# Kernel optimization log

Hardware: AMD Instinct MI355X
Metric: run time of the kernel (lower is better)

The kernel has to match this reference:

```python
import jax, jax.numpy as jnp
import numpy as np

H = 1024      # hidden_size
NH = 16       # num_attention_heads
DK = H // NH  # head dim
C = 1024      # cyclic_size


def setup_inputs() -> dict:
    key = jax.random.key(0)
    ks = jax.random.split(key, 13)
    B, S = 2, 2048
    s = 1.0 / np.sqrt(H)
    inp = {
        "q": jax.random.normal(ks[0], (B, S, H), jnp.float32),
        "k": jax.random.normal(ks[1], (B, S, H), jnp.float32),
        "v": jax.random.normal(ks[2], (B, S, H), jnp.float32),
        "Wq": jax.random.normal(ks[3], (H, H), jnp.float32) * s,
        "bq": jnp.zeros((H,), jnp.float32),
        "Wk": jax.random.normal(ks[4], (H, H), jnp.float32) * s,
        "bk": jnp.zeros((H,), jnp.float32),
        "Wv": jax.random.normal(ks[5], (H, H), jnp.float32) * s,
        "bv": jnp.zeros((H,), jnp.float32),
        "Wo": jax.random.normal(ks[6], (H, H), jnp.float32) * s,
        "bo": jnp.zeros((H,), jnp.float32),
        "Wc": jax.random.normal(ks[7], (H, C), jnp.float32) * s,
        "bc": jnp.zeros((C,), jnp.float32),
    }
    return inp


def _split_heads(x):
    B, S, _ = x.shape
    return x.reshape(B, S, NH, DK).transpose(0, 2, 1, 3)  # [B,NH,S,DK]


def reference(q, k, v, Wq, bq, Wk, bk, Wv, bv, Wo, bo, Wc, bc):
    Q = _split_heads(q @ Wq + bq)
    K = _split_heads(k @ Wk + bk)
    V = _split_heads(v @ Wv + bv)
    # unfused SDPA: full [B,NH,S,S] scores, as in the original module
    scores = jnp.einsum("bhqd,bhkd->bhqk", Q, K) / jnp.sqrt(jnp.float32(DK))
    probs = jax.nn.softmax(scores, axis=-1)
    attn = jnp.einsum("bhqk,bhkd->bhqd", probs, V)  # [B,NH,S,DK]
    B, _, S, _ = attn.shape
    merged = attn.transpose(0, 2, 1, 3).reshape(B, S, H)
    h = merged @ Wo + bo
    c = merged @ Wc + bc
    return (c, h)
```

## Files before the change

kernel.cpp:

```cpp
#include <hip/hip_runtime.h>
#include <stdint.h>

typedef unsigned short u16;
typedef short bf16x8 __attribute__((ext_vector_type(8)));
typedef short bf16x4 __attribute__((ext_vector_type(4)));
typedef float f32x4 __attribute__((ext_vector_type(4)));

#define MB (1u<<20)
#define CL2 0.18033688f

static __device__ __forceinline__ u16 f2bf(float x){
  union { float f; unsigned u; } v; v.f = x;
  return (u16)((v.u + 0x7FFFu + ((v.u >> 16) & 1u)) >> 16);
}

static __device__ __forceinline__ void gld_lds16(const void* g, void* l){
  __builtin_amdgcn_global_load_lds((const __attribute__((address_space(1))) unsigned int*)g,
                                   (__attribute__((address_space(3))) unsigned int*)l, 16, 0, 0);
}

__global__ void convx(const float* __restrict__ q, const float* __restrict__ k, const float* __restrict__ v,
                      u16* __restrict__ qb, u16* __restrict__ kb, u16* __restrict__ vb){
  const float* s = blockIdx.z==0 ? q : (blockIdx.z==1 ? k : v);
  u16* d = blockIdx.z==0 ? qb : (blockIdx.z==1 ? kb : vb);
  int i = (blockIdx.x*256 + threadIdx.x)*4;
  float4 f = *(const float4*)(s + i);
  ushort4 o; o.x=f2bf(f.x); o.y=f2bf(f.y); o.z=f2bf(f.z); o.w=f2bf(f.w);
  *(ushort4*)(d + i) = o;
}

__global__ void convw(const float* W0,const float* W1,const float* W2,const float* W3,const float* W4,
                      u16* T0,u16* T1,u16* T2,u16* T3,u16* T4){
  const float* W = blockIdx.z==0?W0:blockIdx.z==1?W1:blockIdx.z==2?W2:blockIdx.z==3?W3:W4;
  u16* T = blockIdx.z==0?T0:blockIdx.z==1?T1:blockIdx.z==2?T2:blockIdx.z==3?T3:T4;
  __shared__ u16 t[64][65];
  int k0 = blockIdx.x*64, n0 = blockIdx.y*64;
  for (int i=0;i<16;i++){
    int idx = i*256 + threadIdx.x;
    int r = idx >> 6, c = idx & 63;
    t[r][c] = f2bf(W[(size_t)(k0+r)*1024 + n0 + c]);
  }
  __syncthreads();
  for (int i=0;i<2;i++){
    int idx = i*256 + threadIdx.x;
    int nl = idx >> 3, kc = idx & 7;
    bf16x8 o;
    #pragma unroll
    for (int j=0;j<8;j++) o[j] = (short)t[kc*8+j][nl];
    *(bf16x8*)(T + (size_t)(n0+nl)*1024 + k0 + kc*8) = o;
  }
}

template<int MODE>
static __device__ __forceinline__ void gemm_bt_dev(const u16* __restrict__ A, const u16* __restrict__ Bt,
                                                   const float* __restrict__ bias, void* __restrict__ Cout){
  __shared__ u16 As[128*32];
  __shared__ u16 Bs[128*32];
  const int tid = threadIdx.x, lane = tid & 63, w = tid >> 6;
  const int wm = w >> 1, wn = w & 1, quad = lane >> 4, lr = lane & 15;
  const int m0 = blockIdx.y * 128, n0 = blockIdx.x * 128;
  f32x4 acc[4][4] = {};
  const u16* Ab = A + (size_t)m0*1024;
  const u16* Bb = Bt + (size_t)n0*1024;
  const int srow = w*16 + (lane>>2);
  const int sg   = (lane & 3);
  for (int k0 = 0; k0 < 1024; k0 += 32){
    #pragma unroll
    for (int r = 0; r < 2; ++r){
      int row = r*64 + srow;
      int g = sg ^ ((row>>1)&3);
      gld_lds16(Ab + (size_t)row*1024 + k0 + g*8, As + (r*64 + w*16)*32);
      gld_lds16(Bb + (size_t)row*1024 + k0 + g*8, Bs + (r*64 + w*16)*32);
    }
    __syncthreads();
    bf16x8 af[4], bfr[4];
    #pragma unroll
    for (int i=0;i<4;i++){
      int rowa = wm*64 + i*16 + lr;
      af[i] = *(const bf16x8*)(As + rowa*32 + ((quad ^ ((rowa>>1)&3))*8));
      int rowb = wn*64 + i*16 + lr;
      bfr[i] = *(const bf16x8*)(Bs + rowb*32 + ((quad ^ ((rowb>>1)&3))*8));
    }
    #pragma unroll
    for (int mi=0;mi<4;mi++)
      #pragma unroll
      for (int ni=0;ni<4;ni++)
        acc[mi][ni] = __builtin_amdgcn_mfma_f32_16x16x32_bf16(af[mi], bfr[ni], acc[mi][ni], 0, 0, 0);
    __syncthreads();
  }
  #pragma unroll
  for (int mi=0;mi<4;mi++){
    int row = m0 + wm*64 + mi*16 + quad*4;
    #pragma unroll
    for (int ni=0;ni<4;ni++){
      int col = n0 + wn*64 + ni*16 + lr;
      float bb = bias[col];
      #pragma unroll
      for (int rg=0; rg<4; rg++){
        float vv = acc[mi][ni][rg] + bb;
        int r = row + rg;
        if (MODE == 0){
          ((u16*)Cout)[(size_t)r*1024 + col] = f2bf(vv);
        } else if (MODE == 4){
          ((u16*)Cout)[(size_t)r*1024 + col] = f2bf(vv * CL2);
        } else if (MODE == 1){
          ((float*)Cout)[(size_t)r*1024 + col] = vv;
        } else if (MODE == 2){
          int b2 = r >> 11, s = r & 2047, kb2 = s >> 7, kvl = s & 127;
          int hh = col >> 6, hg = (col & 63) >> 3, hl = col & 7;
          ((u16*)Cout)[((size_t)(b2*16+hh)*16 + kb2)*8192 + hg*1024 + kvl*8 + hl] = f2bf(vv);
        } else {
          int b2 = r >> 11, s = r & 2047, kb2 = s >> 7, kvl = s & 127;
          int sgv = kvl >> 2, sl = kvl & 3;
          int hh = col >> 6, dd = col & 63;
          ((u16*)Cout)[((size_t)(b2*16+hh)*16 + kb2)*8192 + sgv*256 + dd*4 + sl] = f2bf(vv);
        }
      }
    }
  }
}

__global__ void qkv_gemm(const u16* qb,const u16* kb,const u16* vb,
                         const u16* Wqt,const u16* Wkt,const u16* Wvt,
                         const float* bq,const float* bk,const float* bv,
                         u16* Qb,u16* Kr,u16* Vr){
  if (blockIdx.z == 0)      gemm_bt_dev<4>(qb, Wqt, bq, Qb);
  else if (blockIdx.z == 1) gemm_bt_dev<2>(kb, Wkt, bk, Kr);
  else                      gemm_bt_dev<3>(vb, Wvt, bv, Vr);
}

__global__ void out_gemm(const u16* Mg, const u16* Wct, const u16* Wot,
                         const float* bc, const float* bo, float* out){
  const u16* B = blockIdx.z==0? Wct : Wot;
  const float* bias = blockIdx.z==0? bc : bo;
  float* C = out + (blockIdx.z==0? 0 : 4194304);
  gemm_bt_dev<1>(Mg, B, bias, C);
}

__global__ __launch_bounds__(512,4) void attn(const u16* __restrict__ Qb, const u16* __restrict__ Kr,
                                              const u16* __restrict__ Vr, u16* __restrict__ Mg){
  __shared__ u16 Ks[2][8192];
  __shared__ u16 Vs[2][8192];
  const int qt = blockIdx.x, bh = blockIdx.y, b = bh >> 4, h = bh & 15;
  const int tid = threadIdx.x, lane = tid & 63, w = tid >> 6;
  const int quad = lane >> 4, lr = lane & 15;
  const int q0 = qt*128 + w*16;

  bf16x8 aq[2];
  #pragma unroll
  for (int ks=0;ks<2;ks++)
    aq[ks] = *(const bf16x8*)(Qb + (size_t)(b*2048 + q0 + lr)*1024 + h*64 + ks*32 + quad*8);

  f32x4 acco[4] = {};
  float lsum = 0.f;

  const u16* Krb = Kr + (size_t)bh*131072;
  const u16* Vrb = Vr + (size_t)bh*131072;

  gld_lds16(Krb + tid*8,        &Ks[0][w*512]);
  gld_lds16(Krb + 4096 + tid*8, &Ks[0][4096 + w*512]);
  gld_lds16(Vrb + tid*8,        &Vs[0][w*512]);
  gld_lds16(Vrb + 4096 + tid*8, &Vs[0][4096 + w*512]);

  for (int kb = 0; kb < 16; kb++){
    __syncthreads();
    const int cur = kb & 1;
    if (kb < 15){
      const u16* kg = Krb + (size_t)(kb+1)*8192;
      const u16* vg = Vrb + (size_t)(kb+1)*8192;
      gld_lds16(kg + tid*8,        &Ks[cur^1][w*512]);
      gld_lds16(kg + 4096 + tid*8, &Ks[cur^1][4096 + w*512]);
      gld_lds16(vg + tid*8,        &Vs[cur^1][w*512]);
      gld_lds16(vg + 4096 + tid*8, &Vs[cur^1][4096 + w*512]);
    }
    const u16* Ksc = Ks[cur];
    const u16* Vsc = Vs[cur];

    f32x4 accs[8] = {};
    #pragma unroll
    for (int ks=0;ks<2;ks++){
      #pragma unroll
      for (int mt=0;mt<8;mt++){
        bf16x8 kf = *(const bf16x8*)(Ksc + (ks*4+quad)*1024 + (mt*16+lr)*8);
        accs[mt] = __builtin_amdgcn_mfma_f32_16x16x32_bf16(kf, aq[ks], accs[mt], 0,0,0);
      }
    }

    bf16x4 pf[8];
    f32x4 psum = {0.f,0.f,0.f,0.f};
    #pragma unroll
    for (int mt=0;mt<8;mt++){
      float p0 = __builtin_amdgcn_exp2f(accs[mt][0]);
      float p1 = __builtin_amdgcn_exp2f(accs[mt][1]);
      float p2 = __builtin_amdgcn_exp2f(accs[mt][2]);
      float p3 = __builtin_amdgcn_exp2f(accs[mt][3]);
      psum[0] += p0; psum[1] += p1; psum[2] += p2; psum[3] += p3;
      unsigned u0 = __float_as_uint(p0) + 0x8000u;
      unsigned u1 = __float_as_uint(p1) + 0x8000u;
      unsigned u2 = __float_as_uint(p2) + 0x8000u;
      unsigned u3 = __float_as_uint(p3) + 0x8000u;
      union { int2 i2; bf16x4 v; } pk;
      pk.i2.x = (int)__builtin_amdgcn_perm(u1, u0, 0x07060302u);
      pk.i2.y = (int)__builtin_amdgcn_perm(u3, u2, 0x07060302u);
      pf[mt] = pk.v;
    }
    lsum += (psum[0] + psum[1]) + (psum[2] + psum[3]);

    #pragma unroll
    for (int dt=0;dt<4;dt++){
      #pragma unroll
      for (int mt=0;mt<8;mt++){
        bf16x4 vf = *(const bf16x4*)(Vsc + (mt*4+quad)*256 + (dt*16+lr)*4);
        acco[dt] = __builtin_amdgcn_mfma_f32_16x16x16bf16_1k(vf, pf[mt], acco[dt], 0,0,0);
      }
    }
  }

  lsum += __shfl_xor(lsum, 16, 64);
  lsum += __shfl_xor(lsum, 32, 64);
  float inv = 1.f / lsum;

  u16* dst = Mg + (size_t)(b*2048 + q0 + lr)*1024 + h*64;
  #pragma unroll
  for (int dt=0;dt<4;dt++){
    bf16x4 o;
    #pragma unroll
    for (int rg=0;rg<4;rg++) o[rg] = (short)f2bf(acco[dt][rg]*inv);
    *(bf16x4*)(dst + dt*16 + quad*4) = o;
  }
}

extern "C" void kernel_launch(void* const* d_in, const int* in_sizes, int n_in,
                              void* d_out, int out_size, void* d_ws, size_t ws_size,
                              hipStream_t stream){
  const float* q  = (const float*)d_in[0];
  const float* k  = (const float*)d_in[1];
  const float* v  = (const float*)d_in[2];
  const float* Wq = (const float*)d_in[3];
  const float* bq = (const float*)d_in[4];
  const float* Wk = (const float*)d_in[5];
  const float* bk = (const float*)d_in[6];
  const float* Wv = (const float*)d_in[7];
  const float* bv = (const float*)d_in[8];
  const float* Wo = (const float*)d_in[9];
  const float* bo = (const float*)d_in[10];
  const float* Wc = (const float*)d_in[11];
  const float* bc = (const float*)d_in[12];
  char* ws = (char*)d_ws;
  u16* qb  = (u16*)(ws + (size_t)0*MB);
  u16* kb  = (u16*)(ws + (size_t)8*MB);
  u16* vb  = (u16*)(ws + (size_t)16*MB);
  u16* Wqt = (u16*)(ws + (size_t)24*MB);
  u16* Wkt = (u16*)(ws + (size_t)26*MB);
  u16* Wvt = (u16*)(ws + (size_t)28*MB);
  u16* Wot = (u16*)(ws + (size_t)30*MB);
  u16* Wct = (u16*)(ws + (size_t)32*MB);
  u16* Qb  = (u16*)(ws + (size_t)34*MB);
  u16* Kr  = (u16*)(ws + (size_t)42*MB);
  u16* Vr  = (u16*)(ws + (size_t)50*MB);
  u16* Mg  = (u16*)(ws + (size_t)58*MB);

  dim3 blk(256,1,1);
  hipLaunchKernelGGL(convx,    dim3(4096,1,3), blk, 0, stream, q,k,v, qb,kb,vb);
  hipLaunchKernelGGL(convw,    dim3(16,16,5),  blk, 0, stream, Wq,Wk,Wv,Wo,Wc, Wqt,Wkt,Wvt,Wot,Wct);
  hipLaunchKernelGGL(qkv_gemm, dim3(8,32,3),   blk, 0, stream, qb,kb,vb, Wqt,Wkt,Wvt, bq,bk,bv, Qb,Kr,Vr);
  hipLaunchKernelGGL(attn,     dim3(16,32,1),  dim3(512,1,1), 0, stream, Qb, Kr, Vr, Mg);
  hipLaunchKernelGGL(out_gemm, dim3(8,32,2),   blk, 0, stream, Mg, Wct, Wot, bc, bo, (float*)d_out);
}
```

Measured before the change: 247.6 us.

## Process two query tiles per wave in attention and sum rows via MFMA

The attention block shrinks from 512 to 256 threads, and each wave now handles 32 query rows as two 16-row tiles instead of one. Each K/V fragment read from shared memory therefore feeds twice as many MFMAs, halving LDS traffic per unit of work. The softmax row sum is no longer a VALU accumulation plus cross-lane shuffles; it comes from an extra MFMA against a vector of ones. The costs are higher register pressure and fewer waves per block to hide latency, and the MFMA row sum is taken over the bf16-rounded probabilities rather than the fp32 values.

```diff
diff --git a/kernel.cpp b/kernel.cpp
--- a/kernel.cpp
+++ b/kernel.cpp
@@ -137,30 +137,34 @@
   gemm_bt_dev<1>(Mg, B, bias, C);
 }
 
-__global__ __launch_bounds__(512,4) void attn(const u16* __restrict__ Qb, const u16* __restrict__ Kr,
+__global__ __launch_bounds__(256,2) void attn(const u16* __restrict__ Qb, const u16* __restrict__ Kr,
                                               const u16* __restrict__ Vr, u16* __restrict__ Mg){
   __shared__ u16 Ks[2][8192];
   __shared__ u16 Vs[2][8192];
   const int qt = blockIdx.x, bh = blockIdx.y, b = bh >> 4, h = bh & 15;
   const int tid = threadIdx.x, lane = tid & 63, w = tid >> 6;
   const int quad = lane >> 4, lr = lane & 15;
-  const int q0 = qt*128 + w*16;
-
-  bf16x8 aq[2];
-  #pragma unroll
-  for (int ks=0;ks<2;ks++)
-    aq[ks] = *(const bf16x8*)(Qb + (size_t)(b*2048 + q0 + lr)*1024 + h*64 + ks*32 + quad*8);
-
-  f32x4 acco[4] = {};
-  float lsum = 0.f;
+  const int q0 = qt*128 + w*32;
+
+  bf16x8 aq[2][2];
+  #pragma unroll
+  for (int t=0;t<2;t++)
+    #pragma unroll
+    for (int ks=0;ks<2;ks++)
+      aq[t][ks] = *(const bf16x8*)(Qb + (size_t)(b*2048 + q0 + t*16 + lr)*1024 + h*64 + ks*32 + quad*8);
+
+  f32x4 acco[2][4] = {};
+  f32x4 accl[2] = {};
+  const bf16x4 ones = {(short)0x3F80,(short)0x3F80,(short)0x3F80,(short)0x3F80};
 
   const u16* Krb = Kr + (size_t)bh*131072;
   const u16* Vrb = Vr + (size_t)bh*131072;
 
-  gld_lds16(Krb + tid*8,        &Ks[0][w*512]);
-  gld_lds16(Krb + 4096 + tid*8, &Ks[0][4096 + w*512]);
-  gld_lds16(Vrb + tid*8,        &Vs[0][w*512]);
-  gld_lds16(Vrb + 4096 + tid*8, &Vs[0][4096 + w*512]);
+  #pragma unroll
+  for (int j=0;j<4;j++){
+    gld_lds16(Krb + j*2048 + tid*8, &Ks[0][j*2048 + w*512]);
+    gld_lds16(Vrb + j*2048 + tid*8, &Vs[0][j*2048 + w*512]);
+  }
 
   for (int kb = 0; kb < 16; kb++){
     __syncthreads();
@@ -168,65 +172,74 @@
     if (kb < 15){
       const u16* kg = Krb + (size_t)(kb+1)*8192;
       const u16* vg = Vrb + (size_t)(kb+1)*8192;
-      gld_lds16(kg + tid*8,        &Ks[cur^1][w*512]);
-      gld_lds16(kg + 4096 + tid*8, &Ks[cur^1][4096 + w*512]);
-      gld_lds16(vg + tid*8,        &Vs[cur^1][w*512]);
-      gld_lds16(vg + 4096 + tid*8, &Vs[cur^1][4096 + w*512]);
+      #pragma unroll
+      for (int j=0;j<4;j++){
+        gld_lds16(kg + j*2048 + tid*8, &Ks[cur^1][j*2048 + w*512]);
+        gld_lds16(vg + j*2048 + tid*8, &Vs[cur^1][j*2048 + w*512]);
+      }
     }
     const u16* Ksc = Ks[cur];
     const u16* Vsc = Vs[cur];
 
-    f32x4 accs[8] = {};
+    f32x4 accs[2][8] = {};
     #pragma unroll
     for (int ks=0;ks<2;ks++){
       #pragma unroll
       for (int mt=0;mt<8;mt++){
         bf16x8 kf = *(const bf16x8*)(Ksc + (ks*4+quad)*1024 + (mt*16+lr)*8);
-        accs[mt] = __builtin_amdgcn_mfma_f32_16x16x32_bf16(kf, aq[ks], accs[mt], 0,0,0);
-      }
-    }
-
-    bf16x4 pf[8];
-    f32x4 psum = {0.f,0.f,0.f,0.f};
+        accs[0][mt] = __builtin_amdgcn_mfma_f32_16x16x32_bf16(kf, aq[0][ks], accs[0][mt], 0,0,0);
+        accs[1][mt] = __builtin_amdgcn_mfma_f32_16x16x32_bf16(kf, aq[1][ks], accs[1][mt], 0,0,0);
+      }
+    }
+
+    bf16x4 pf[2][8];
+    #pragma unroll
+    for (int t=0;t<2;t++){
+      #pragma unroll
+      for (int mt=0;mt<8;mt++){
+        float p0 = __builtin_amdgcn_exp2f(accs[t][mt][0]);
+        float p1 = __builtin_amdgcn_exp2f(accs[t][mt][1]);
+        float p2 = __builtin_amdgcn_exp2f(accs[t][mt][2]);
+        float p3 = __builtin_amdgcn_exp2f(accs[t][mt][3]);
+        unsigned u0 = __float_as_uint(p0) + 0x8000u;
+        unsigned u1 = __float_as_uint(p1) + 0x8000u;
+        unsigned u2 = __float_as_uint(p2) + 0x8000u;
+        unsigned u3 = __float_as_uint(p3) + 0x8000u;
+        union { int2 i2; bf16x4 v; } pk;
+        pk.i2.x = (int)__builtin_amdgcn_perm(u1, u0, 0x07060302u);
+        pk.i2.y = (int)__builtin_amdgcn_perm(u3, u2, 0x07060302u);
+        pf[t][mt] = pk.v;
+      }
+    }
+
     #pragma unroll
     for (int mt=0;mt<8;mt++){
-      float p0 = __builtin_amdgcn_exp2f(accs[mt][0]);
-      float p1 = __builtin_amdgcn_exp2f(accs[mt][1]);
-      float p2 = __builtin_amdgcn_exp2f(accs[mt][2]);
-      float p3 = __builtin_amdgcn_exp2f(accs[mt][3]);
-      psum[0] += p0; psum[1] += p1; psum[2] += p2; psum[3] += p3;
-      unsigned u0 = __float_as_uint(p0) + 0x8000u;
-      unsigned u1 = __float_as_uint(p1) + 0x8000u;
-      unsigned u2 = __float_as_uint(p2) + 0x8000u;
-      unsigned u3 = __float_as_uint(p3) + 0x8000u;
-      union { int2 i2; bf16x4 v; } pk;
-      pk.i2.x = (int)__builtin_amdgcn_perm(u1, u0, 0x07060302u);
-      pk.i2.y = (int)__builtin_amdgcn_perm(u3, u2, 0x07060302u);
-      pf[mt] = pk.v;
-    }
-    lsum += (psum[0] + psum[1]) + (psum[2] + psum[3]);
+      accl[0] = __builtin_amdgcn_mfma_f32_16x16x16bf16_1k(ones, pf[0][mt], accl[0], 0,0,0);
+      accl[1] = __builtin_amdgcn_mfma_f32_16x16x16bf16_1k(ones, pf[1][mt], accl[1], 0,0,0);
+    }
 
     #pragma unroll
     for (int dt=0;dt<4;dt++){
       #pragma unroll
       for (int mt=0;mt<8;mt++){
         bf16x4 vf = *(const bf16x4*)(Vsc + (mt*4+quad)*256 + (dt*16+lr)*4);
-        acco[dt] = __builtin_amdgcn_mfma_f32_16x16x16bf16_1k(vf, pf[mt], acco[dt], 0,0,0);
-      }
-    }
-  }
-
-  lsum += __shfl_xor(lsum, 16, 64);
-  lsum += __shfl_xor(lsum, 32, 64);
-  float inv = 1.f / lsum;
-
-  u16* dst = Mg + (size_t)(b*2048 + q0 + lr)*1024 + h*64;
-  #pragma unroll
-  for (int dt=0;dt<4;dt++){
-    bf16x4 o;
-    #pragma unroll
-    for (int rg=0;rg<4;rg++) o[rg] = (short)f2bf(acco[dt][rg]*inv);
-    *(bf16x4*)(dst + dt*16 + quad*4) = o;
+        acco[0][dt] = __builtin_amdgcn_mfma_f32_16x16x16bf16_1k(vf, pf[0][mt], acco[0][dt], 0,0,0);
+        acco[1][dt] = __builtin_amdgcn_mfma_f32_16x16x16bf16_1k(vf, pf[1][mt], acco[1][dt], 0,0,0);
+      }
+    }
+  }
+
+  #pragma unroll
+  for (int t=0;t<2;t++){
+    float inv = 1.f / accl[t][0];
+    u16* dst = Mg + (size_t)(b*2048 + q0 + t*16 + lr)*1024 + h*64;
+    #pragma unroll
+    for (int dt=0;dt<4;dt++){
+      bf16x4 o;
+      #pragma unroll
+      for (int rg=0;rg<4;rg++) o[rg] = (short)f2bf(acco[t][dt][rg]*inv);
+      *(bf16x4*)(dst + dt*16 + quad*4) = o;
+    }
   }
 }
 
@@ -264,6 +277,6 @@
   hipLaunchKernelGGL(convx,    dim3(4096,1,3), blk, 0, stream, q,k,v, qb,kb,vb);
   hipLaunchKernelGGL(convw,    dim3(16,16,5),  blk, 0, stream, Wq,Wk,Wv,Wo,Wc, Wqt,Wkt,Wvt,Wot,Wct);
   hipLaunchKernelGGL(qkv_gemm, dim3(8,32,3),   blk, 0, stream, qb,kb,vb, Wqt,Wkt,Wvt, bq,bk,bv, Qb,Kr,Vr);
-  hipLaunchKernelGGL(attn,     dim3(16,32,1),  dim3(512,1,1), 0, stream, Qb, Kr, Vr, Mg);
+  hipLaunchKernelGGL(attn,     dim3(16,32,1),  blk, 0, stream, Qb, Kr, Vr, Mg);
   hipLaunchKernelGGL(out_gemm, dim3(8,32,2),   blk, 0, stream, Mg, Wct, Wot, bc, bo, (float*)d_out);
 }
```

Result: no change. 243.2 us (-1.8%).
